# Kernel tuning notes

Hardware: AMD Instinct MI355X
Metric: run time of the kernel (lower is better)

Reference implementation:

```python
import jax, jax.numpy as jnp
import numpy as np

WS = 7      # window size
SS = 3      # shift size = WS // 2
NH = 12     # num heads
EPS = 1e-5  # LayerNorm eps


def _ln(x, g, b):
    m = jnp.mean(x, axis=-1, keepdims=True)
    v = jnp.var(x, axis=-1, keepdims=True)
    return (x - m) * jax.lax.rsqrt(v + EPS) * g + b


def _rel_index(ws):
    # relative position index (N, N), N = ws*ws (static, numpy)
    coords = np.stack(np.meshgrid(np.arange(ws), np.arange(ws), indexing='ij')).reshape(2, -1)
    rel = (coords[:, :, None] - coords[:, None, :]).transpose(1, 2, 0).copy()
    rel[:, :, 0] += ws - 1
    rel[:, :, 1] += ws - 1
    rel[:, :, 0] *= 2 * ws - 1
    return rel.sum(-1)


def _attn_mask(H, W, ws, ss):
    # SW-MSA mask (nW, N, N): -100 where tokens come from different shifted regions
    img = np.zeros((H, W), np.float32)
    cnt = 0
    sls = (slice(0, -ws), slice(-ws, -ss), slice(-ss, None))
    for hs in sls:
        for wsl in sls:
            img[hs, wsl] = cnt
            cnt += 1
    win = img.reshape(H // ws, ws, W // ws, ws).transpose(0, 2, 1, 3).reshape(-1, ws * ws)
    d = win[:, None, :] - win[:, :, None]
    return np.where(d != 0, -100.0, 0.0).astype(np.float32)


def _forward(x, rel_bias_table, qkv_w, qkv_b, proj_w, proj_b,
             norm1_w, norm1_b, norm2_w, norm2_b,
             mlp_w1, mlp_b1, mlp_w2, mlp_b2, h, w):
    B, L, C = x.shape
    ws, ss, nH = WS, SS, NH
    hd = C // nH
    N = ws * ws
    scale = hd ** -0.5
    nWh, nWw = h // ws, w // ws
    nW = nWh * nWw

    shortcut = x
    y = _ln(x, norm1_w, norm1_b).reshape(B, h, w, C)
    # cyclic shift (SW-MSA)
    y = jnp.roll(y, (-ss, -ss), axis=(1, 2))
    # window partition -> (B*nW, N, C)
    y = y.reshape(B, nWh, ws, nWw, ws, C).transpose(0, 1, 3, 2, 4, 5).reshape(-1, N, C)

    qkv = (y @ qkv_w + qkv_b).reshape(-1, N, 3, nH, hd).transpose(2, 0, 3, 1, 4)
    q, k, v = qkv[0] * scale, qkv[1], qkv[2]  # (Bw, nH, N, hd)

    attn = jnp.einsum('bhnd,bhmd->bhnm', q, k)  # (Bw, nH, N, N)
    # learned relative position bias
    idx = jnp.asarray(_rel_index(ws))  # (N, N)
    bias = rel_bias_table[idx].transpose(2, 0, 1)[None]  # (1, nH, N, N)
    attn = attn + bias
    # shifted-window mask
    mask = jnp.asarray(_attn_mask(h, w, ws, ss))  # (nW, N, N)
    attn = attn.reshape(B, nW, nH, N, N) + mask[None, :, None]
    attn = jax.nn.softmax(attn.reshape(-1, nH, N, N), axis=-1)

    out = jnp.einsum('bhnm,bhmd->bhnd', attn, v).transpose(0, 2, 1, 3).reshape(-1, N, C)
    out = out @ proj_w + proj_b
    # window reverse + un-shift
    out = out.reshape(B, nWh, nWw, ws, ws, C).transpose(0, 1, 3, 2, 4, 5).reshape(B, h, w, C)
    out = jnp.roll(out, (ss, ss), axis=(1, 2)).reshape(B, L, C)

    x = shortcut + out
    y2 = _ln(x, norm2_w, norm2_b)
    mlp = jax.nn.gelu(y2 @ mlp_w1 + mlp_b1, approximate=False) @ mlp_w2 + mlp_b2
    return x + mlp


def setup_inputs() -> dict:
    key = jax.random.key(0)
    ks = jax.random.split(key, 8)
    B, H, W, C = 32, 56, 56, 384
    hid = int(C * 4.0)
    ws, nH = WS, NH
    inp = {
        'x': jax.random.normal(ks[0], (B, H * W, C), jnp.float32),
        'rel_bias_table': 0.02 * jax.random.normal(ks[1], ((2 * ws - 1) * (2 * ws - 1), nH), jnp.float32),
        'qkv_w': 0.02 * jax.random.normal(ks[2], (C, 3 * C), jnp.float32),
        'qkv_b': jnp.zeros((3 * C,), jnp.float32),
        'proj_w': 0.02 * jax.random.normal(ks[3], (C, C), jnp.float32),
        'proj_b': jnp.zeros((C,), jnp.float32),
        'norm1_w': jnp.ones((C,), jnp.float32),
        'norm1_b': jnp.zeros((C,), jnp.float32),
        'norm2_w': jnp.ones((C,), jnp.float32),
        'norm2_b': jnp.zeros((C,), jnp.float32),
        'mlp_w1': 0.02 * jax.random.normal(ks[4], (C, hid), jnp.float32),
        'mlp_b1': jnp.zeros((hid,), jnp.float32),
        'mlp_w2': 0.02 * jax.random.normal(ks[5], (hid, C), jnp.float32),
        'mlp_b2': jnp.zeros((C,), jnp.float32),
        'h': H,
        'w': W,
    }
    return inp


def reference(x, rel_bias_table, qkv_w, qkv_b, proj_w, proj_b,
              norm1_w, norm1_b, norm2_w, norm2_b,
              mlp_w1, mlp_b1, mlp_w2, mlp_b2, h, w):
    return _forward(x, rel_bias_table, qkv_w, qkv_b, proj_w, proj_b,
                    norm1_w, norm1_b, norm2_w, norm2_b,
                    mlp_w1, mlp_b1, mlp_w2, mlp_b2, h, w)
```

## Files before the change

### kernel.cpp

```cpp
#include <hip/hip_runtime.h>

typedef unsigned short u16;
typedef unsigned int u32;
typedef short s8v __attribute__((ext_vector_type(8)));
typedef float f4 __attribute__((ext_vector_type(4)));

#define GL16(g, l) __builtin_amdgcn_global_load_lds((const __attribute__((address_space(1))) u32*)(g), (__attribute__((address_space(3))) u32*)(l), 16, 0, 0)

__device__ __forceinline__ u16 f2bf(float f){
  u32 u = __builtin_bit_cast(u32, f);
  u32 r = u + 0x7fffu + ((u >> 16) & 1u);
  return (u16)(r >> 16);
}
__device__ __forceinline__ float bf2f(u16 u){
  u32 x = ((u32)u) << 16;
  return __builtin_bit_cast(float, x);
}

__device__ __forceinline__ u32 pk_bf16(float lo, float hi){
  u32 r;
  asm("v_cvt_pk_bf16_f32 %0, %1, %2" : "=v"(r) : "v"(lo), "v"(hi));
  return r;
}

__device__ __forceinline__ float gelu_f(float x){
  float y = fabsf(x) * 0.70710678118654752f;
  float t = __builtin_amdgcn_rcpf(1.f + 0.3275911f*y);
  float p = ((((1.061405429f*t - 1.453152027f)*t + 1.421413741f)*t - 0.284496736f)*t + 0.254829592f)*t;
  float er = 1.f - p*__expf(-y*y);
  er = copysignf(er, x);
  return 0.5f*x*(1.f + er);
}

__device__ __forceinline__ int win_to_src(int orow){
  int wi = orow / 49;
  int n  = orow - wi*49;
  int b  = wi >> 6;
  int wq = wi & 63;
  int wh = wq >> 3, ww = wq & 7;
  int r = n / 7, c = n - r*7;
  int hh = wh*7 + r + 3; if (hh >= 56) hh -= 56;
  int wp = ww*7 + c + 3; if (wp >= 56) wp -= 56;
  return (b*56 + hh)*56 + wp;
}

__global__ void sentinel_kernel(float* o){ o[0] = 1.0e9f; }

__global__ void transpose_cast(const float* __restrict__ in, u16* __restrict__ out,
                               int K, int N, float scale, int scale_lim){
  __shared__ float tile[16][17];
  int kb = blockIdx.x*16, nb = blockIdx.y*16;
  int tx = threadIdx.x, ty = threadIdx.y;
  int k = kb + ty, n = nb + tx;
  tile[ty][tx] = (k < K && n < N) ? in[(size_t)k*N + n] : 0.f;
  __syncthreads();
  int on = nb + ty, ok = kb + tx;
  if (on < N && ok < K){
    float v = tile[tx][ty];
    if (on < scale_lim) v *= scale;
    out[(size_t)on*K + ok] = f2bf(v);
  }
}

__global__ void scale_bias(const float* __restrict__ in, float* __restrict__ out,
                           int n, float s, int lim){
  int i = blockIdx.x*256 + threadIdx.x;
  if (i < n) out[i] = in[i] * (i < lim ? s : 1.f);
}

__global__ void build_biasmask(const float* __restrict__ table, u16* __restrict__ bm){
  int wq = blockIdx.x, h = blockIdx.y;
  int wh = wq >> 3, ww = wq & 7;
  u16* o = bm + (size_t)(wq*12 + h) * 4096;
  for (int i = threadIdx.x; i < 4096; i += 256){
    int m = i >> 6, n = i & 63;
    float v;
    if (m < 49 && n < 49){
      int rm = m/7, cm = m - rm*7;
      int rn = n/7, cn = n - rn*7;
      int idx = (rm - rn + 6)*13 + (cm - cn + 6);
      v = table[idx*12 + h];
      int ym = wh*7 + rm, xm = ww*7 + cm;
      int yn = wh*7 + rn, xn = ww*7 + cn;
      int lm = (ym < 49 ? 0 : (ym < 53 ? 1 : 2))*3 + (xm < 49 ? 0 : (xm < 53 ? 1 : 2));
      int ln = (yn < 49 ? 0 : (yn < 53 ? 1 : 2))*3 + (xn < 49 ? 0 : (xn < 53 ? 1 : 2));
      if (lm != ln) v += -100.f;
    } else {
      v = -1e9f;
    }
    o[i] = f2bf(v);
  }
}

template<bool GATHER>
__global__ __launch_bounds__(256) void ln_kernel(const float* __restrict__ x,
    const float* __restrict__ g, const float* __restrict__ b,
    u16* __restrict__ y, int nrows)
{
  int row = blockIdx.x*4 + (threadIdx.x >> 6);
  int lane = threadIdx.x & 63;
  if (row >= nrows) return;
  int src = GATHER ? win_to_src(row) : row;
  const float* xr = x + (size_t)src*384;
  float v[6];
  float s = 0.f, s2 = 0.f;
  #pragma unroll
  for (int p = 0; p < 3; p++){
    float2 t = *(const float2*)(xr + p*128 + lane*2);
    v[p*2] = t.x; v[p*2+1] = t.y;
    s += t.x + t.y; s2 += t.x*t.x + t.y*t.y;
  }
  #pragma unroll
  for (int off = 32; off; off >>= 1){
    s  += __shfl_xor(s,  off);
    s2 += __shfl_xor(s2, off);
  }
  float mean = s * (1.f/384.f);
  float var  = s2 * (1.f/384.f) - mean*mean;
  float rs   = rsqrtf(var + 1e-5f);
  u16* yr = y + (size_t)row*384;
  #pragma unroll
  for (int p = 0; p < 3; p++){
    int c = p*128 + lane*2;
    float a0 = (v[p*2]   - mean)*rs*g[c]   + b[c];
    float a1 = (v[p*2+1] - mean)*rs*g[c+1] + b[c+1];
    *(u32*)(yr + c) = pk_bf16(a0, a1);
  }
}

template<int MODE, int NF>
__global__ __launch_bounds__(256) void gemm_bf16(
    const u16* __restrict__ A, const u16* __restrict__ Bt,
    const float* __restrict__ bias, const float* __restrict__ resid,
    void* __restrict__ outp, int K, int N, int gn)
{
  constexpr int TN = NF * 32;
  __shared__ u16 As[2][128*64];
  __shared__ u16 Bs[2][TN*64];
  const int tid  = threadIdx.x;
  const int lane = tid & 63, wv = tid >> 6;
  const int wr = wv >> 1, wc = wv & 1;
  const int l15 = lane & 15, lhi = lane >> 4;
  const int sw  = l15 & 7;

  int total = gridDim.x;
  int flat  = blockIdx.x;
  int swz   = flat;
  if ((total & 7) == 0){
    int cpx = total >> 3;
    swz = (flat & 7)*cpx + (flat >> 3);
  }
  int bm = swz / gn, bn = swz - bm*gn;
  const size_t m0 = (size_t)bm * 128;
  const int n0 = bn * TN;

  f4 acc[4][NF] = {};

  auto stage = [&](int buf, int kt){
    #pragma unroll
    for (int it = 0; it < 4; it++){
      int c = it*256 + tid;
      int row = c >> 3;
      int col = (((c & 7) ^ (row & 7))) * 8;
      const u16* ga = A + (m0 + (size_t)row)*K + kt*64 + col;
      GL16(ga, &As[buf][(it*256 + wv*64)*8]);
    }
    #pragma unroll
    for (int it = 0; it < NF; it++){
      int c = it*256 + tid;
      int row = c >> 3;
      int col = (((c & 7) ^ (row & 7))) * 8;
      const u16* gb = Bt + ((size_t)n0 + row)*K + kt*64 + col;
      GL16(gb, &Bs[buf][(it*256 + wv*64)*8]);
    }
  };

  const int nk = K >> 6;
  stage(0, 0);
  for (int kt = 0; kt < nk; kt++){
    const int cur = kt & 1;
    if (kt + 1 < nk){
      stage(cur ^ 1, kt + 1);
      asm volatile("s_waitcnt vmcnt(8)" ::: "memory");
    } else {
      asm volatile("s_waitcnt vmcnt(0)" ::: "memory");
    }
    __builtin_amdgcn_s_barrier();
    #pragma unroll
    for (int kk = 0; kk < 2; kk++){
      s8v a[4], bb[NF];
      #pragma unroll
      for (int mi = 0; mi < 4; mi++)
        a[mi] = *(const s8v*)&As[cur][(wr*64 + mi*16 + l15)*64 + ((kk*4 + lhi) ^ sw)*8];
      #pragma unroll
      for (int ni = 0; ni < NF; ni++)
        bb[ni] = *(const s8v*)&Bs[cur][(wc*NF*16 + ni*16 + l15)*64 + ((kk*4 + lhi) ^ sw)*8];
      #pragma unroll
      for (int mi = 0; mi < 4; mi++)
        #pragma unroll
        for (int ni = 0; ni < NF; ni++)
          acc[mi][ni] = __builtin_amdgcn_mfma_f32_16x16x32_bf16(bb[ni], a[mi], acc[mi][ni], 0, 0, 0);
    }
    asm volatile("s_waitcnt lgkmcnt(0)" ::: "memory");
    __builtin_amdgcn_s_barrier();
  }

  if constexpr (MODE == 0 || MODE == 2){
    u16* tile = (u16*)&As[0][0];
    #pragma unroll
    for (int mi = 0; mi < 4; mi++){
      int ml = wr*64 + mi*16 + l15;
      #pragma unroll
      for (int ni = 0; ni < NF; ni++){
        int nl = wc*NF*16 + ni*16 + lhi*4;
        f4 v = acc[mi][ni];
        float4 b4 = *(const float4*)(bias + n0 + nl);
        v[0] += b4.x; v[1] += b4.y; v[2] += b4.z; v[3] += b4.w;
        u32 p0, p1;
        if constexpr (MODE == 2){
          p0 = pk_bf16(gelu_f(v[0]), gelu_f(v[1]));
          p1 = pk_bf16(gelu_f(v[2]), gelu_f(v[3]));
        } else {
          p0 = pk_bf16(v[0], v[1]);
          p1 = pk_bf16(v[2], v[3]);
        }
        *(u32*)&tile[ml*136 + nl]     = p0;
        *(u32*)&tile[ml*136 + nl + 2] = p1;
      }
    }
    __syncthreads();
    int rr = tid >> 4;
    int cc = (tid & 15) * 8;
    #pragma unroll
    for (int pass = 0; pass < 8; pass++){
      int row = rr + pass*16;
      uint4 val = *(const uint4*)&tile[row*136 + cc];
      *(uint4*)((u16*)outp + ((size_t)((int)m0 + row))*N + n0 + cc) = val;
    }
  } else {
    #pragma unroll
    for (int mi = 0; mi < 4; mi++){
      int m = (int)m0 + wr*64 + mi*16 + l15;
      int src = 0;
      if constexpr (MODE == 1) src = win_to_src(m);
      #pragma unroll
      for (int ni = 0; ni < NF; ni++){
        int n = n0 + wc*NF*16 + ni*16 + lhi*4;
        f4 v = acc[mi][ni];
        float4 b4 = *(const float4*)(bias + n);
        v[0] += b4.x; v[1] += b4.y; v[2] += b4.z; v[3] += b4.w;
        if constexpr (MODE == 1){
          const float4 r4 = *(const float4*)(resid + (size_t)src*384 + n);
          float4 o4; o4.x = v[0]+r4.x; o4.y = v[1]+r4.y; o4.z = v[2]+r4.z; o4.w = v[3]+r4.w;
          *(float4*)((float*)outp + (size_t)src*384 + n) = o4;
        } else {
          float4* o = (float4*)((float*)outp + (size_t)m*N + n);
          float4 c4 = *o;
          c4.x += v[0]; c4.y += v[1]; c4.z += v[2]; c4.w += v[3];
          *o = c4;
        }
      }
    }
  }
}

__global__ __launch_bounds__(256) void attn_kernel(
    const u16* __restrict__ qkv, const u16* __restrict__ bm, u16* __restrict__ ao)
{
  const int wi = blockIdx.x;
  const int hg = blockIdx.y;
  const int wv = threadIdx.x >> 6, lane = threadIdx.x & 63;
  const int h = hg*4 + wv;
  const int l15 = lane & 15, lhi = lane >> 4;
  const int wq = wi & 63;

  __shared__ u16 Plds[4][64*72];
  __shared__ u16 Vlds[4][32*72];

  const size_t base = (size_t)wi * 49 * 1152;
  s8v z8 = (s8v)0;

  #pragma unroll
  for (int i = 0; i < 4; i++){
    int n  = i*16 + (lane >> 2);
    int d8 = (lane & 3)*8;
    s8v v = (n < 49) ? *(const s8v*)&qkv[base + (size_t)n*1152 + 768 + h*32 + d8] : z8;
    #pragma unroll
    for (int j = 0; j < 8; j++)
      Vlds[wv][(d8 + j)*72 + n] = (u16)v[j];
  }

  s8v aQ[4], bK[4];
  #pragma unroll
  for (int mi = 0; mi < 4; mi++){
    int rowq = mi*16 + l15;
    aQ[mi] = (rowq < 49) ? *(const s8v*)&qkv[base + (size_t)rowq*1152 +   0 + h*32 + lhi*8] : z8;
    bK[mi] = (rowq < 49) ? *(const s8v*)&qkv[base + (size_t)rowq*1152 + 384 + h*32 + lhi*8] : z8;
  }
  f4 zf = {0.f, 0.f, 0.f, 0.f};
  f4 s[4][4];
  #pragma unroll
  for (int mi = 0; mi < 4; mi++)
    #pragma unroll
    for (int ni = 0; ni < 4; ni++)
      s[mi][ni] = __builtin_amdgcn_mfma_f32_16x16x32_bf16(aQ[mi], bK[ni], zf, 0, 0, 0);

  const u16* bmp = bm + (size_t)(wq*12 + h) * 4096;
  #pragma unroll
  for (int mi = 0; mi < 4; mi++)
    #pragma unroll
    for (int ni = 0; ni < 4; ni++)
      #pragma unroll
      for (int r = 0; r < 4; r++){
        int m = mi*16 + lhi*4 + r, n = ni*16 + l15;
        s[mi][ni][r] += bf2f(bmp[m*64 + n]);
      }

  #pragma unroll
  for (int mi = 0; mi < 4; mi++){
    #pragma unroll
    for (int r = 0; r < 4; r++){
      float mx = fmaxf(fmaxf(s[mi][0][r], s[mi][1][r]), fmaxf(s[mi][2][r], s[mi][3][r]));
      mx = fmaxf(mx, __shfl_xor(mx, 1));
      mx = fmaxf(mx, __shfl_xor(mx, 2));
      mx = fmaxf(mx, __shfl_xor(mx, 4));
      mx = fmaxf(mx, __shfl_xor(mx, 8));
      float sum = 0.f;
      #pragma unroll
      for (int ni = 0; ni < 4; ni++){
        float p = __expf(s[mi][ni][r] - mx);
        s[mi][ni][r] = p; sum += p;
      }
      sum += __shfl_xor(sum, 1);
      sum += __shfl_xor(sum, 2);
      sum += __shfl_xor(sum, 4);
      sum += __shfl_xor(sum, 8);
      float inv = 1.f / sum;
      #pragma unroll
      for (int ni = 0; ni < 4; ni++) s[mi][ni][r] *= inv;
    }
  }

  #pragma unroll
  for (int mi = 0; mi < 4; mi++)
    #pragma unroll
    for (int ni = 0; ni < 4; ni++)
      #pragma unroll
      for (int r = 0; r < 4; r++){
        int m = mi*16 + lhi*4 + r, n = ni*16 + l15;
        Plds[wv][m*72 + n] = f2bf(s[mi][ni][r]);
      }
  __syncthreads();

  f4 o[4][2] = {};
  #pragma unroll
  for (int ks = 0; ks < 2; ks++){
    s8v aP[4], bV[2];
    #pragma unroll
    for (int mi = 0; mi < 4; mi++)
      aP[mi] = *(const s8v*)&Plds[wv][(mi*16 + l15)*72 + ks*32 + lhi*8];
    #pragma unroll
    for (int di = 0; di < 2; di++)
      bV[di] = *(const s8v*)&Vlds[wv][(di*16 + l15)*72 + ks*32 + lhi*8];
    #pragma unroll
    for (int mi = 0; mi < 4; mi++)
      #pragma unroll
      for (int di = 0; di < 2; di++)
        o[mi][di] = __builtin_amdgcn_mfma_f32_16x16x32_bf16(aP[mi], bV[di], o[mi][di], 0, 0, 0);
  }

  #pragma unroll
  for (int mi = 0; mi < 4; mi++)
    #pragma unroll
    for (int di = 0; di < 2; di++)
      #pragma unroll
      for (int r = 0; r < 4; r++){
        int m = mi*16 + lhi*4 + r;
        if (m < 49){
          int d = di*16 + l15;
          ao[((size_t)wi*49 + m)*384 + h*32 + d] = f2bf(o[mi][di][r]);
        }
      }
}

extern "C" void kernel_launch(void* const* d_in, const int* in_sizes, int n_in,
                              void* d_out, int out_size, void* d_ws, size_t ws_size,
                              hipStream_t stream)
{
  const float* x      = (const float*)d_in[0];
  const float* table  = (const float*)d_in[1];
  const float* qkv_w  = (const float*)d_in[2];
  const float* qkv_b  = (const float*)d_in[3];
  const float* proj_w = (const float*)d_in[4];
  const float* proj_b = (const float*)d_in[5];
  const float* n1w    = (const float*)d_in[6];
  const float* n1b    = (const float*)d_in[7];
  const float* n2w    = (const float*)d_in[8];
  const float* n2b    = (const float*)d_in[9];
  const float* w1     = (const float*)d_in[10];
  const float* b1     = (const float*)d_in[11];
  const float* w2     = (const float*)d_in[12];
  const float* b2     = (const float*)d_in[13];
  float* out = (float*)d_out;

  const size_t M = 100352;
  const float SC = 0.17677669529663689f;

  const size_t R1 = M * 1536 * 2;
  const size_t R2 = M * 384 * 2;
  const size_t R3 = (size_t)64*12*64*64*2;
  const size_t WT = (size_t)(1152*384 + 384*384 + 1536*384 + 384*1536) * 2;
  const size_t BB = 1152 * 4;
  const size_t needed = R1 + R2 + R3 + WT + BB;
  if (ws_size < needed){
    sentinel_kernel<<<1, 1, 0, stream>>>(out);
    return;
  }

  char* p = (char*)d_ws;
  u16*   qkvbuf = (u16*)p;
  u16*   ybuf   = (u16*)(p + R1);
  u16*   bmbuf  = (u16*)(p + R1 + R2);
  u16*   qkvT   = (u16*)(p + R1 + R2 + R3);
  u16*   projT  = qkvT  + (size_t)1152*384;
  u16*   w1T    = projT + (size_t)384*384;
  u16*   w2T    = w1T   + (size_t)1536*384;
  float* qkvb_s = (float*)(p + R1 + R2 + R3 + WT);

  transpose_cast<<<dim3(24, 72),  dim3(16,16), 0, stream>>>(qkv_w,  qkvT, 384, 1152, SC, 384);
  transpose_cast<<<dim3(24, 24),  dim3(16,16), 0, stream>>>(proj_w, projT, 384, 384, 1.f, 0);
  transpose_cast<<<dim3(24, 96),  dim3(16,16), 0, stream>>>(w1,     w1T,  384, 1536, 1.f, 0);
  transpose_cast<<<dim3(96, 24),  dim3(16,16), 0, stream>>>(w2,     w2T,  1536, 384, 1.f, 0);
  scale_bias<<<5, 256, 0, stream>>>(qkv_b, qkvb_s, 1152, SC, 384);
  build_biasmask<<<dim3(64, 12), 256, 0, stream>>>(table, bmbuf);

  ln_kernel<true><<<M/4, 256, 0, stream>>>(x, n1w, n1b, ybuf, (int)M);

  gemm_bf16<0,4><<<784*9, 256, 0, stream>>>(ybuf, qkvT, qkvb_s, nullptr, qkvbuf, 384, 1152, 9);

  attn_kernel<<<dim3(2048, 3), 256, 0, stream>>>(qkvbuf, bmbuf, ybuf);

  gemm_bf16<1,4><<<784*3, 256, 0, stream>>>(ybuf, projT, proj_b, x, out, 384, 384, 3);

  ln_kernel<false><<<M/4, 256, 0, stream>>>(out, n2w, n2b, ybuf, (int)M);

  gemm_bf16<2,4><<<784*12, 256, 0, stream>>>(ybuf, w1T, b1, nullptr, qkvbuf, 384, 1536, 12);

  gemm_bf16<3,4><<<784*3, 256, 0, stream>>>(qkvbuf, w2T, b2, nullptr, out, 1536, 384, 3);
}
```

Before: 969.5 us.

## Switch GEMM to triple-buffered LDS pipeline with 32-wide K tiles

The bf16 GEMM main loop moves from double buffering 64-wide K tiles to triple buffering 32-wide K tiles, prefetching two stages ahead. The LDS swizzle is reworked for 32-element rows, and the A/B buffers are merged into one 48KB shared array instead of 64KB. The aim is to hide global-load latency better and lower LDS use so more blocks can be resident. The cost is twice as many barriers per unit of K. The B staging loop is now fixed at two iterations, which assumes NF=4.

```diff
diff --git a/kernel.cpp b/kernel.cpp
--- a/kernel.cpp
+++ b/kernel.cpp
@@ -135,13 +135,12 @@
     void* __restrict__ outp, int K, int N, int gn)
 {
   constexpr int TN = NF * 32;
-  __shared__ u16 As[2][128*64];
-  __shared__ u16 Bs[2][TN*64];
+  __shared__ u16 smem[6*4096];
   const int tid  = threadIdx.x;
   const int lane = tid & 63, wv = tid >> 6;
   const int wr = wv >> 1, wc = wv & 1;
   const int l15 = lane & 15, lhi = lane >> 4;
-  const int sw  = l15 & 7;
+  const int key = (l15 >> 1) & 3;
 
   int total = gridDim.x;
   int flat  = blockIdx.x;
@@ -158,55 +157,59 @@
 
   auto stage = [&](int buf, int kt){
     #pragma unroll
-    for (int it = 0; it < 4; it++){
+    for (int it = 0; it < 2; it++){
       int c = it*256 + tid;
-      int row = c >> 3;
-      int col = (((c & 7) ^ (row & 7))) * 8;
-      const u16* ga = A + (m0 + (size_t)row)*K + kt*64 + col;
-      GL16(ga, &As[buf][(it*256 + wv*64)*8]);
-    }
-    #pragma unroll
-    for (int it = 0; it < NF; it++){
+      int row = c >> 2;
+      int col = ((c & 3) ^ ((c >> 3) & 3)) * 8;
+      const u16* ga = A + (m0 + (size_t)row)*K + kt*32 + col;
+      GL16(ga, &smem[buf*4096 + (it*256 + wv*64)*8]);
+    }
+    #pragma unroll
+    for (int it = 0; it < 2; it++){
       int c = it*256 + tid;
-      int row = c >> 3;
-      int col = (((c & 7) ^ (row & 7))) * 8;
-      const u16* gb = Bt + ((size_t)n0 + row)*K + kt*64 + col;
-      GL16(gb, &Bs[buf][(it*256 + wv*64)*8]);
+      int row = c >> 2;
+      int col = ((c & 3) ^ ((c >> 3) & 3)) * 8;
+      const u16* gb = Bt + ((size_t)n0 + row)*K + kt*32 + col;
+      GL16(gb, &smem[12288 + buf*4096 + (it*256 + wv*64)*8]);
     }
   };
 
-  const int nk = K >> 6;
+  const int nk = K >> 5;
   stage(0, 0);
+  stage(1, 1);
+  int cur = 0;
   for (int kt = 0; kt < nk; kt++){
-    const int cur = kt & 1;
-    if (kt + 1 < nk){
-      stage(cur ^ 1, kt + 1);
+    if (kt + 2 < nk){
+      int nb = cur + 2; if (nb >= 3) nb -= 3;
+      stage(nb, kt + 2);
       asm volatile("s_waitcnt vmcnt(8)" ::: "memory");
+    } else if (kt + 1 < nk){
+      asm volatile("s_waitcnt vmcnt(4)" ::: "memory");
     } else {
       asm volatile("s_waitcnt vmcnt(0)" ::: "memory");
     }
     __builtin_amdgcn_s_barrier();
-    #pragma unroll
-    for (int kk = 0; kk < 2; kk++){
-      s8v a[4], bb[NF];
-      #pragma unroll
-      for (int mi = 0; mi < 4; mi++)
-        a[mi] = *(const s8v*)&As[cur][(wr*64 + mi*16 + l15)*64 + ((kk*4 + lhi) ^ sw)*8];
+
+    s8v a[4], bb[NF];
+    #pragma unroll
+    for (int mi = 0; mi < 4; mi++)
+      a[mi] = *(const s8v*)&smem[cur*4096 + (wr*64 + mi*16 + l15)*32 + ((lhi ^ key))*8];
+    #pragma unroll
+    for (int ni = 0; ni < NF; ni++)
+      bb[ni] = *(const s8v*)&smem[12288 + cur*4096 + (wc*NF*16 + ni*16 + l15)*32 + ((lhi ^ key))*8];
+    #pragma unroll
+    for (int mi = 0; mi < 4; mi++)
       #pragma unroll
       for (int ni = 0; ni < NF; ni++)
-        bb[ni] = *(const s8v*)&Bs[cur][(wc*NF*16 + ni*16 + l15)*64 + ((kk*4 + lhi) ^ sw)*8];
-      #pragma unroll
-      for (int mi = 0; mi < 4; mi++)
-        #pragma unroll
-        for (int ni = 0; ni < NF; ni++)
-          acc[mi][ni] = __builtin_amdgcn_mfma_f32_16x16x32_bf16(bb[ni], a[mi], acc[mi][ni], 0, 0, 0);
-    }
+        acc[mi][ni] = __builtin_amdgcn_mfma_f32_16x16x32_bf16(bb[ni], a[mi], acc[mi][ni], 0, 0, 0);
+
     asm volatile("s_waitcnt lgkmcnt(0)" ::: "memory");
     __builtin_amdgcn_s_barrier();
+    cur = (cur == 2) ? 0 : cur + 1;
   }
 
   if constexpr (MODE == 0 || MODE == 2){
-    u16* tile = (u16*)&As[0][0];
+    u16* tile = smem;
     #pragma unroll
     for (int mi = 0; mi < 4; mi++){
       int ml = wr*64 + mi*16 + l15;
```

Result: faster. 941.2 us (-2.9%).
